# Optimization experiments

Hardware: AMD Instinct MI355X
Metric: run time of the kernel (lower is better)

## Reference

```python
import jax, jax.numpy as jnp
import numpy as np

B, K, D = 262144, 512, 3


def setup_inputs() -> dict:
    key = jax.random.key(0)
    k_ze, k_e = jax.random.split(key)
    ze = jax.random.normal(k_ze, (B, D, 1), dtype=jnp.float32)
    e = jax.random.normal(k_e, (K, D), dtype=jnp.float32)  # codebook, learned param
    return {"ze": ze, "e": e}


def reference(ze, e):
    # ze: (B, D, 1), e: (K, D)
    # Per-dimension L2 distance to every codebook entry: (B, K, D)
    l2diff = (jnp.transpose(ze, (0, 2, 1)) - e[None, :, :]) ** 2
    # Independent argmin over the codebook axis for each of the D dims: (B, D)
    z = jnp.argmin(l2diff, axis=1)
    # Gather per-dimension codebook scalars: zq[b, d] = e[z[b, d], d]
    zq = e[z, jnp.arange(D)]  # (B, D)
    return (z, zq)
```

## Files before the change

kernel.cpp:

```cpp
#include <hip/hip_runtime.h>

#define B_TOTAL 262144
#define K_CB    512
#define D_DIM   3
#define BLOCK   256

__device__ __forceinline__ unsigned int mono32(unsigned int u) {
    unsigned int m = (u & 0x80000000u) ? 0xFFFFFFFFu : 0x80000000u;
    return u ^ m;
}

__global__ __launch_bounds__(BLOCK) void rank_kernel(
    const float* __restrict__ e, float* __restrict__ ws_val, int* __restrict__ ws_idx)
{
    const int d    = blockIdx.x >> 1;
    const int half = blockIdx.x & 1;
    const int tid  = threadIdx.x;

    __shared__ unsigned long long key[K_CB];
    __shared__ float              val[K_CB];

    for (int k = tid; k < K_CB; k += BLOCK) {
        float v = e[k * D_DIM + d];
        key[k] = ((unsigned long long)mono32(__float_as_uint(v)) << 32) | (unsigned int)k;
        val[k] = v;
    }
    __syncthreads();

    const int i = half * BLOCK + tid;
    const unsigned long long mykey = key[i];
    int rank = 0;
    #pragma unroll 8
    for (int j = 0; j < K_CB; ++j)
        rank += (key[j] < mykey) ? 1 : 0;

    ws_val[d * K_CB + rank] = val[i];
    ws_idx[d * K_CB + rank] = i;
}

__global__ __launch_bounds__(BLOCK) void vq_search_kernel(
    const float* __restrict__ ze,
    const float* __restrict__ ws_val, const int* __restrict__ ws_idx,
    float* __restrict__ z_out, float* __restrict__ zq_out)
{
    __shared__ float sval[D_DIM][K_CB];
    __shared__ int   sidx[D_DIM][K_CB];

    const int tid = threadIdx.x;
    {
        const float4* gv = (const float4*)ws_val; float4* lv = (float4*)sval;
        for (int i = tid; i < D_DIM * K_CB / 4; i += BLOCK) lv[i] = gv[i];
        const int4*   gi = (const int4*)ws_idx;   int4*   li = (int4*)sidx;
        for (int i = tid; i < D_DIM * K_CB / 4; i += BLOCK) li[i] = gi[i];
    }
    __syncthreads();

    const int b = blockIdx.x * BLOCK + tid;
    const float xs[D_DIM] = { ze[b * 3 + 0], ze[b * 3 + 1], ze[b * 3 + 2] };

    #pragma unroll
    for (int d = 0; d < D_DIM; ++d) {
        const float xv = xs[d];

        int lo = -1, hi = K_CB;
        #pragma unroll
        for (int it = 0; it < 10; ++it) {
            int mid = (lo + hi) >> 1;
            bool le = sval[d][mid] <= xv;
            lo = le ? mid : lo;
            hi = le ? hi : mid;
        }

        float dl = 3.402823466e38f, vl = 0.0f; int il = 0;
        if (lo >= 0) {
            vl = sval[d][lo];
            int p = lo;
            while (p > 0 && sval[d][p - 1] == vl) --p;
            il = sidx[d][p];
            float t = xv - vl;
            dl = t * t;
        }
        float dr = 3.402823466e38f, vr = 0.0f; int ir = 0;
        if (lo < K_CB - 1) {
            vr = sval[d][lo + 1];
            ir = sidx[d][lo + 1];
            float t = xv - vr;
            dr = t * t;
        }

        const bool pickR = (dr < dl) || ((dr == dl) && (ir < il));
        z_out [b * 3 + d] = (float)(pickR ? ir : il);
        zq_out[b * 3 + d] = pickR ? vr : vl;
    }
}

extern "C" void kernel_launch(void* const* d_in, const int* in_sizes, int n_in,
                              void* d_out, int out_size, void* d_ws, size_t ws_size,
                              hipStream_t stream) {
    const float* ze = (const float*)d_in[0];
    const float* e  = (const float*)d_in[1];
    float* z_out  = (float*)d_out;
    float* zq_out = z_out + (size_t)B_TOTAL * D_DIM;

    float* ws_val = (float*)d_ws;
    int*   ws_idx = (int*)(ws_val + D_DIM * K_CB);

    rank_kernel     <<<D_DIM * 2,       BLOCK, 0, stream>>>(e, ws_val, ws_idx);
    vq_search_kernel<<<B_TOTAL / BLOCK, BLOCK, 0, stream>>>(ze, ws_val, ws_idx,
                                                            z_out, zq_out);
}
```

Before: 70.29 us.

## Process flattened scalars as float4 with sentinel-padded sorted codebook

The search kernel now treats ze and the outputs as a flat array of B*3 scalars. Each thread loads and stores one float4 and computes each element's dimension from its flat index, which replaces stride-3 scalar accesses with coalesced vector accesses. The rank kernel precomputes the smallest original index among equal values, so the backward tie-scan loop disappears. Sentinel entries pad both ends of the sorted table so no boundary branches are needed. Per-thread dimension selection adds some divergence in shared-memory indexing.

```diff
diff --git a/kernel.cpp b/kernel.cpp
--- a/kernel.cpp
+++ b/kernel.cpp
@@ -4,6 +4,8 @@
 #define K_CB    512
 #define D_DIM   3
 #define BLOCK   256
+#define NSCAL   (B_TOTAL * D_DIM)
+#define SLEN    (K_CB + 2)
 
 __device__ __forceinline__ unsigned int mono32(unsigned int u) {
     unsigned int m = (u & 0x80000000u) ? 0xFFFFFFFFu : 0x80000000u;
@@ -29,69 +31,78 @@
 
     const int i = half * BLOCK + tid;
     const unsigned long long mykey = key[i];
+    const unsigned int       myv   = (unsigned int)(mykey >> 32);
     int rank = 0;
+    unsigned int minIdx = 0xFFFFFFFFu;
     #pragma unroll 8
-    for (int j = 0; j < K_CB; ++j)
-        rank += (key[j] < mykey) ? 1 : 0;
+    for (int j = 0; j < K_CB; ++j) {
+        unsigned long long kj = key[j];
+        rank += (kj < mykey) ? 1 : 0;
+        if ((unsigned int)(kj >> 32) == myv)
+            minIdx = min(minIdx, (unsigned int)kj);
+    }
 
     ws_val[d * K_CB + rank] = val[i];
-    ws_idx[d * K_CB + rank] = i;
+    ws_idx[d * K_CB + rank] = (int)minIdx;
 }
 
 __global__ __launch_bounds__(BLOCK) void vq_search_kernel(
-    const float* __restrict__ ze,
+    const float4* __restrict__ ze4,
     const float* __restrict__ ws_val, const int* __restrict__ ws_idx,
-    float* __restrict__ z_out, float* __restrict__ zq_out)
+    float4* __restrict__ z4, float4* __restrict__ zq4)
 {
-    __shared__ float sval[D_DIM][K_CB];
-    __shared__ int   sidx[D_DIM][K_CB];
+    __shared__ float sval [D_DIM][SLEN];
+    __shared__ int   shead[D_DIM][SLEN];
 
     const int tid = threadIdx.x;
-    {
-        const float4* gv = (const float4*)ws_val; float4* lv = (float4*)sval;
-        for (int i = tid; i < D_DIM * K_CB / 4; i += BLOCK) lv[i] = gv[i];
-        const int4*   gi = (const int4*)ws_idx;   int4*   li = (int4*)sidx;
-        for (int i = tid; i < D_DIM * K_CB / 4; i += BLOCK) li[i] = gi[i];
+    for (int i = tid; i < D_DIM * K_CB; i += BLOCK) {
+        const int d = i >> 9, k = i & (K_CB - 1);
+        sval [d][k + 1] = ws_val[i];
+        shead[d][k + 1] = ws_idx[i];
+    }
+    if (tid < D_DIM) {
+        sval [tid][0]        = -3.402823466e38f;
+        sval [tid][K_CB + 1] =  3.402823466e38f;
+        shead[tid][0]        = 0x7FFFFFFF;
+        shead[tid][K_CB + 1] = 0x7FFFFFFF;
     }
     __syncthreads();
 
-    const int b = blockIdx.x * BLOCK + tid;
-    const float xs[D_DIM] = { ze[b * 3 + 0], ze[b * 3 + 1], ze[b * 3 + 2] };
+    const int gid = blockIdx.x * BLOCK + tid;
+    const float4 x = ze4[gid];
+    const float xs[4] = { x.x, x.y, x.z, x.w };
+    const int d0 = gid % 3;
 
+    float zf[4], zqf[4];
     #pragma unroll
-    for (int d = 0; d < D_DIM; ++d) {
-        const float xv = xs[d];
+    for (int j = 0; j < 4; ++j) {
+        int dj = d0 + j;
+        if (dj >= 3) dj -= 3;
+        const float* __restrict__ sv = sval [dj];
+        const int*   __restrict__ sh = shead[dj];
+        const float xv = xs[j];
 
-        int lo = -1, hi = K_CB;
+        int lo = 0, hi = K_CB + 1;
         #pragma unroll
         for (int it = 0; it < 10; ++it) {
-            int mid = (lo + hi) >> 1;
-            bool le = sval[d][mid] <= xv;
+            const int mid = (lo + hi) >> 1;
+            const bool le = sv[mid] <= xv;
             lo = le ? mid : lo;
             hi = le ? hi : mid;
         }
 
-        float dl = 3.402823466e38f, vl = 0.0f; int il = 0;
-        if (lo >= 0) {
-            vl = sval[d][lo];
-            int p = lo;
-            while (p > 0 && sval[d][p - 1] == vl) --p;
-            il = sidx[d][p];
-            float t = xv - vl;
-            dl = t * t;
-        }
-        float dr = 3.402823466e38f, vr = 0.0f; int ir = 0;
-        if (lo < K_CB - 1) {
-            vr = sval[d][lo + 1];
-            ir = sidx[d][lo + 1];
-            float t = xv - vr;
-            dr = t * t;
-        }
+        const float vl = sv[lo],     vr = sv[lo + 1];
+        const int   il = sh[lo],     ir = sh[lo + 1];
+        const float tl = xv - vl,    tr = xv - vr;
+        const float dl = tl * tl,    dr = tr * tr;
 
         const bool pickR = (dr < dl) || ((dr == dl) && (ir < il));
-        z_out [b * 3 + d] = (float)(pickR ? ir : il);
-        zq_out[b * 3 + d] = pickR ? vr : vl;
+        zf [j] = (float)(pickR ? ir : il);
+        zqf[j] = pickR ? vr : vl;
     }
+
+    z4 [gid] = make_float4(zf[0],  zf[1],  zf[2],  zf[3]);
+    zq4[gid] = make_float4(zqf[0], zqf[1], zqf[2], zqf[3]);
 }
 
 extern "C" void kernel_launch(void* const* d_in, const int* in_sizes, int n_in,
@@ -105,7 +116,7 @@
     float* ws_val = (float*)d_ws;
     int*   ws_idx = (int*)(ws_val + D_DIM * K_CB);
 
-    rank_kernel     <<<D_DIM * 2,       BLOCK, 0, stream>>>(e, ws_val, ws_idx);
-    vq_search_kernel<<<B_TOTAL / BLOCK, BLOCK, 0, stream>>>(ze, ws_val, ws_idx,
-                                                            z_out, zq_out);
+    rank_kernel<<<D_DIM * 2, BLOCK, 0, stream>>>(e, ws_val, ws_idx);
+    vq_search_kernel<<<NSCAL / 4 / BLOCK, BLOCK, 0, stream>>>(
+        (const float4*)ze, ws_val, ws_idx, (float4*)z_out, (float4*)zq_out);
 }
```

Result: slower. 74.01 us (+5.3%).
